# Performance work log

Measured on AMD Instinct MI355X. Metric: run time of the kernel, lower is better.

The kernel has to match this reference:

```python
import math
import jax, jax.numpy as jnp
import numpy as np

NUM_TIERS = 3
TIER_SIZE = 50
GT_FACTOR = 2.0
MAX_REL = 8  # upper bound on relevant (gt) docs per query; labels built to respect this
B, D = 4096, 1000


def diff_fn(x):
    # 'maxmargin': relu(1 - x)
    return jax.nn.relu(1.0 - x)


def get_tier_inds(num_negatives):
    # tier_distance is None -> auto-spread tier centers
    mids = math.ceil((num_negatives - 2 * TIER_SIZE) / (NUM_TIERS - 1))
    return [0] + [TIER_SIZE // 2 + i * mids for i in range(1, NUM_TIERS - 1)] + [num_negatives - TIER_SIZE]


def setup_inputs() -> dict:
    key = jax.random.key(0)
    k1, k2 = jax.random.split(key)
    scores = jax.random.normal(k1, (B, D), dtype=jnp.float32)
    # n_i relevant docs per query in [1, MAX_REL]; labels[i,:n_i] = positions, rest -1
    n = jax.random.randint(k2, (B,), 1, MAX_REL + 1)
    cols = jnp.arange(D)
    labels = jnp.where(cols[None, :] < n[:, None], cols[None, :], -1).astype(jnp.int32)
    return {"scores": scores, "labels": labels}


def reference(scores, labels):
    Bq, Dq = scores.shape
    start_inds = get_tier_inds(Dq)
    loss = jnp.zeros(Bq, dtype=jnp.float32)
    # tiered pairwise diffs: each tier vs everything below it
    for t in range(NUM_TIERS - 1):
        s1 = scores[:, start_inds[t]:start_inds[t] + TIER_SIZE]      # (B, tier_size)
        s2 = scores[:, start_inds[t + 1]:]                            # (B, rest)
        d = diff_fn(s1[:, :, None] - s2[:, None, :])                  # (B, tier_size, rest)
        loss = loss + jnp.sum(d, axis=(1, 2)) / (s1.shape[1] * s2.shape[1])
    # ground-truth component (gt_function='same'), vectorized with masks instead of per-row loop
    n = jnp.sum(labels > -1, axis=1)                                  # (B,) num relevant per query
    rel_mask = jnp.arange(MAX_REL)[None, :] < n[:, None]              # (B, MAX_REL): j < n_i
    neg_mask = jnp.arange(Dq)[None, :] >= n[:, None]                  # (B, D): k >= n_i
    d = diff_fn(scores[:, :MAX_REL, None] - scores[:, None, :])       # (B, MAX_REL, D)
    mask = rel_mask[:, :, None] & neg_mask[:, None, :]
    gt_loss = jnp.sum(jnp.where(mask, d, 0.0), axis=(1, 2)) / Dq      # (B,)
    loss = loss + GT_FACTOR * gt_loss
    return jnp.mean(loss)  # reduction='mean'
```

## Files before the change

kernel.cpp:

```cpp
#include <hip/hip_runtime.h>


#define BQ 4096
#define DQ 1000

__global__ __launch_bounds__(256) void mtl_row_kernel(const float* __restrict__ scores,
                                                      const int* __restrict__ labels,
                                                      float* __restrict__ row_loss) {
    const int row = blockIdx.x;
    __shared__ float s[DQ];
    __shared__ int n_sh;
    __shared__ float wsum[4];

    const float* sr = scores + (size_t)row * DQ;
    for (int j = threadIdx.x; j < DQ; j += 256) s[j] = sr[j];

    if (threadIdx.x == 0) {
        const int* lr = labels + (size_t)row * DQ;
        int n = 0;
        #pragma unroll
        for (int k = 0; k < 8; ++k) n += (lr[k] > -1) ? 1 : 0;
        n_sh = n;
    }
    __syncthreads();
    const int n = n_sh;

    float acc = 0.0f;
    for (int j = threadIdx.x; j < DQ; j += 256) {
        const float sj = s[j];
        if (j >= 475) {
            float t = 0.0f;
            #pragma unroll 10
            for (int i = 0; i < 50; ++i) t += fmaxf(1.0f - s[i] + sj, 0.0f);
            acc += t * (1.0f / 26250.0f);
        }
        if (j >= 950) {
            float t = 0.0f;
            #pragma unroll 10
            for (int i = 475; i < 525; ++i) t += fmaxf(1.0f - s[i] + sj, 0.0f);
            acc += t * (1.0f / 2500.0f);
        }
        if (j >= n) {
            float t = 0.0f;
            for (int k = 0; k < n; ++k) t += fmaxf(1.0f - s[k] + sj, 0.0f);
            acc += t * (2.0f / 1000.0f);
        }
    }

    #pragma unroll
    for (int off = 32; off > 0; off >>= 1) acc += __shfl_down(acc, off, 64);
    const int lane = threadIdx.x & 63;
    const int wid  = threadIdx.x >> 6;
    if (lane == 0) wsum[wid] = acc;
    __syncthreads();
    if (threadIdx.x == 0) row_loss[row] = wsum[0] + wsum[1] + wsum[2] + wsum[3];
}

__global__ __launch_bounds__(256) void mtl_reduce_kernel(const float* __restrict__ row_loss,
                                                         float* __restrict__ out) {
    __shared__ float wsum[4];
    float acc = 0.0f;
    for (int i = threadIdx.x; i < BQ; i += 256) acc += row_loss[i];
    #pragma unroll
    for (int off = 32; off > 0; off >>= 1) acc += __shfl_down(acc, off, 64);
    const int lane = threadIdx.x & 63;
    const int wid  = threadIdx.x >> 6;
    if (lane == 0) wsum[wid] = acc;
    __syncthreads();
    if (threadIdx.x == 0) out[0] = (wsum[0] + wsum[1] + wsum[2] + wsum[3]) * (1.0f / (float)BQ);
}

extern "C" void kernel_launch(void* const* d_in, const int* in_sizes, int n_in,
                              void* d_out, int out_size, void* d_ws, size_t ws_size,
                              hipStream_t stream) {
    const float* scores = (const float*)d_in[0];
    const int*   labels = (const int*)d_in[1];
    float* row_loss = (float*)d_ws;
    float* out = (float*)d_out;

    mtl_row_kernel<<<BQ, 256, 0, stream>>>(scores, labels, row_loss);
    mtl_reduce_kernel<<<1, 256, 0, stream>>>(row_loss, out);
}
```

Baseline: 92.33 us.

## Replace tier-0 pairwise hinge sum with sort, prefix sums and binary search

The 50 tier-0 scores are sorted with a rank-based sort in one wavefront and prefix-summed, so each of the 525 lower documents gets its hinge contribution from a binary search plus one prefix lookup instead of a 50-term loop. The remaining tier-1 and ground-truth work is redistributed across the other three wavefronts, and row loads use float4. This removes most of the O(50·525) arithmetic per row. In exchange it adds extra barriers, idle lanes during the sort, and a different float summation order.

```diff
diff --git a/kernel.cpp b/kernel.cpp
--- a/kernel.cpp
+++ b/kernel.cpp
@@ -1,4 +1,5 @@
 #include <hip/hip_runtime.h>
+#include <float.h>
 
 
 #define BQ 4096
@@ -7,15 +8,24 @@
 __global__ __launch_bounds__(256) void mtl_row_kernel(const float* __restrict__ scores,
                                                       const int* __restrict__ labels,
                                                       float* __restrict__ row_loss) {
-    const int row = blockIdx.x;
+    const int row  = blockIdx.x;
+    const int tid  = threadIdx.x;
+    const int lane = tid & 63;
+    const int wid  = tid >> 6;
+
     __shared__ float s[DQ];
-    __shared__ int n_sh;
+    __shared__ float sorted0[64];
+    __shared__ float pre0[65];
+    __shared__ int   n_sh;
     __shared__ float wsum[4];
 
     const float* sr = scores + (size_t)row * DQ;
-    for (int j = threadIdx.x; j < DQ; j += 256) s[j] = sr[j];
-
-    if (threadIdx.x == 0) {
+    if (tid < 250) {
+        float4 v = ((const float4*)sr)[tid];
+        s[tid * 4 + 0] = v.x; s[tid * 4 + 1] = v.y;
+        s[tid * 4 + 2] = v.z; s[tid * 4 + 3] = v.w;
+    }
+    if (tid == 0) {
         const int* lr = labels + (size_t)row * DQ;
         int n = 0;
         #pragma unroll
@@ -26,34 +36,69 @@
     const int n = n_sh;
 
     float acc = 0.0f;
-    for (int j = threadIdx.x; j < DQ; j += 256) {
-        const float sj = s[j];
-        if (j >= 475) {
-            float t = 0.0f;
-            #pragma unroll 10
-            for (int i = 0; i < 50; ++i) t += fmaxf(1.0f - s[i] + sj, 0.0f);
-            acc += t * (1.0f / 26250.0f);
+
+    if (wid == 0) {
+        if (lane >= 50) sorted0[lane] = FLT_MAX;
+        else {
+            float v = s[lane];
+            int rank = 0;
+            for (int k = 0; k < 50; ++k) {
+                float sk = s[k];
+                rank += (sk < v || (sk == v && k < lane)) ? 1 : 0;
+            }
+            sorted0[rank] = v;
         }
-        if (j >= 950) {
-            float t = 0.0f;
-            #pragma unroll 10
-            for (int i = 475; i < 525; ++i) t += fmaxf(1.0f - s[i] + sj, 0.0f);
-            acc += t * (1.0f / 2500.0f);
+    } else {
+        float sj = s[950 + (lane < 50 ? lane : 0)];
+        float t1 = 0.0f;
+        for (int i = wid - 1; i < 50; i += 3) {
+            float ri = s[475 + i];
+            t1 += fmaxf(1.0f - ri + sj, 0.0f);
         }
-        if (j >= n) {
-            float t = 0.0f;
-            for (int k = 0; k < n; ++k) t += fmaxf(1.0f - s[k] + sj, 0.0f);
-            acc += t * (2.0f / 1000.0f);
+        if (lane < 50) acc += t1 * (1.0f / 2500.0f);
+
+        float tgt = 0.0f;
+        for (int j = tid - 64; j < DQ; j += 192) {
+            if (j >= n) {
+                float x = 1.0f + s[j];
+                float t = 0.0f;
+                for (int k = 0; k < n; ++k)
+                    t += fmaxf(x - s[k], 0.0f);
+                tgt += t;
+            }
         }
+        acc += tgt * (2.0f / 1000.0f);
     }
+    __syncthreads();
+
+    if (wid == 0) {
+        float val = (lane < 50) ? sorted0[lane] : 0.0f;
+        #pragma unroll
+        for (int off = 1; off < 64; off <<= 1) {
+            float tmp = __shfl_up(val, off, 64);
+            if (lane >= off) val += tmp;
+        }
+        pre0[lane + 1] = val;
+        if (lane == 0) pre0[0] = 0.0f;
+    }
+    __syncthreads();
+
+    float t0 = 0.0f;
+    for (int j = 475 + tid; j < DQ; j += 256) {
+        float x = 1.0f + s[j];
+        int c = 0;
+        #pragma unroll
+        for (int st = 32; st >= 1; st >>= 1)
+            c += (sorted0[c + st - 1] < x) ? st : 0;
+        t0 += (float)c * x - pre0[c];
+    }
+    acc += t0 * (1.0f / 26250.0f);
 
     #pragma unroll
     for (int off = 32; off > 0; off >>= 1) acc += __shfl_down(acc, off, 64);
-    const int lane = threadIdx.x & 63;
-    const int wid  = threadIdx.x >> 6;
     if (lane == 0) wsum[wid] = acc;
     __syncthreads();
-    if (threadIdx.x == 0) row_loss[row] = wsum[0] + wsum[1] + wsum[2] + wsum[3];
+    if (tid == 0) row_loss[row] = wsum[0] + wsum[1] + wsum[2] + wsum[3];
 }
 
 __global__ __launch_bounds__(256) void mtl_reduce_kernel(const float* __restrict__ row_loss,
```

New measurement: 88.39 us. 4.3% less time.

## Replace tier pairwise loops with sorted prefix-sum relu sums, one wave per row

Applied to the files above, without the earlier changes.

Each wave now handles one row, holding the row in registers instead of shared memory. The two 50-element tier windows are sorted with a wave-level bitonic sort and prefix-summed. Each relu sum against a tier then becomes a binary search plus a count-times-value minus prefix lookup, replacing the 50-iteration inner loops. This removes most of the O(50·D) arithmetic and the block-level syncs, but adds shuffle-heavy sort, scan and search steps and hard-codes the tier boundaries into lane and register masks.

```diff
diff --git a/kernel.cpp b/kernel.cpp
--- a/kernel.cpp
+++ b/kernel.cpp
@@ -1,59 +1,107 @@
 #include <hip/hip_runtime.h>
+#include <float.h>
 
 
 #define BQ 4096
 #define DQ 1000
 
-__global__ __launch_bounds__(256) void mtl_row_kernel(const float* __restrict__ scores,
-                                                      const int* __restrict__ labels,
-                                                      float* __restrict__ row_loss) {
-    const int row = blockIdx.x;
-    __shared__ float s[DQ];
-    __shared__ int n_sh;
-    __shared__ float wsum[4];
+__device__ __forceinline__ float bitonic_sort64(float v, int lane) {
+    #pragma unroll
+    for (int size = 2; size <= 64; size <<= 1) {
+        #pragma unroll
+        for (int stride = size >> 1; stride > 0; stride >>= 1) {
+            float other = __shfl_xor(v, stride, 64);
+            bool keep_min = (((lane & stride) == 0) == ((lane & size) == 0));
+            v = keep_min ? fminf(v, other) : fmaxf(v, other);
+        }
+    }
+    return v;
+}
 
+__device__ __forceinline__ float excl_scan50(float sv, int lane) {
+    float x = (lane < 50) ? sv : 0.0f;
+    float inc = x;
+    #pragma unroll
+    for (int off = 1; off < 64; off <<= 1) {
+        float t = __shfl_up(inc, off, 64);
+        if (lane >= off) inc += t;
+    }
+    return inc - x;
+}
+
+__device__ __forceinline__ float sorted_relu_sum(float x, float sv, float pre) {
+    int c = 0;
+    #pragma unroll
+    for (int st = 32; st >= 1; st >>= 1) {
+        float scv = __shfl(sv, c + st - 1, 64);
+        c += (scv < x) ? st : 0;
+    }
+    float p = __shfl(pre, c, 64);
+    return (float)c * x - p;
+}
+
+__global__ __launch_bounds__(256) void mtl_rows(const float* __restrict__ scores,
+                                               const int* __restrict__ labels,
+                                               float* __restrict__ row_loss) {
+    const int tid  = threadIdx.x;
+    const int lane = tid & 63;
+    const int w    = tid >> 6;
+    const int row  = blockIdx.x * 4 + w;
     const float* sr = scores + (size_t)row * DQ;
-    for (int j = threadIdx.x; j < DQ; j += 256) s[j] = sr[j];
 
-    if (threadIdx.x == 0) {
-        const int* lr = labels + (size_t)row * DQ;
-        int n = 0;
+    float q[16];
+    #pragma unroll
+    for (int t = 0; t < 15; ++t) q[t] = sr[lane + 64 * t];
+    q[15] = (lane < 40) ? sr[960 + lane] : 0.0f;
+
+    int lv = -1;
+    if (lane < 8) lv = labels[(size_t)row * DQ + lane];
+    const int n = __popcll(__ballot(lv > -1));
+
+    float sv0  = bitonic_sort64((lane < 50) ? q[0] : FLT_MAX, lane);
+    float pre0 = excl_scan50(sv0, lane);
+
+    float r1 = FLT_MAX;
+    if (lane < 50) r1 = sr[475 + lane];
+    float sv1  = bitonic_sort64(r1, lane);
+    float pre1 = excl_scan50(sv1, lane);
+
+    float tgt[16];
+    #pragma unroll
+    for (int t = 0; t < 16; ++t) tgt[t] = 0.0f;
+    for (int k = 0; k < n; ++k) {
+        float gk = 1.0f - __shfl(q[0], k, 64);
         #pragma unroll
-        for (int k = 0; k < 8; ++k) n += (lr[k] > -1) ? 1 : 0;
-        n_sh = n;
+        for (int t = 0; t < 16; ++t) tgt[t] += fmaxf(q[t] + gk, 0.0f);
     }
-    __syncthreads();
-    const int n = n_sh;
+    float gts = (lane >= n) ? tgt[0] : 0.0f;
+    #pragma unroll
+    for (int t = 1; t < 15; ++t) gts += tgt[t];
+    gts += (lane < 40) ? tgt[15] : 0.0f;
+    float acc = gts * (2.0f / 1000.0f);
 
-    float acc = 0.0f;
-    for (int j = threadIdx.x; j < DQ; j += 256) {
-        const float sj = s[j];
-        if (j >= 475) {
-            float t = 0.0f;
-            #pragma unroll 10
-            for (int i = 0; i < 50; ++i) t += fmaxf(1.0f - s[i] + sj, 0.0f);
-            acc += t * (1.0f / 26250.0f);
-        }
-        if (j >= 950) {
-            float t = 0.0f;
-            #pragma unroll 10
-            for (int i = 475; i < 525; ++i) t += fmaxf(1.0f - s[i] + sj, 0.0f);
-            acc += t * (1.0f / 2500.0f);
-        }
-        if (j >= n) {
-            float t = 0.0f;
-            for (int k = 0; k < n; ++k) t += fmaxf(1.0f - s[k] + sj, 0.0f);
-            acc += t * (2.0f / 1000.0f);
-        }
+    float t0s = 0.0f;
+    #pragma unroll
+    for (int t = 7; t < 16; ++t) {
+        float x = 1.0f + q[t];
+        float val = sorted_relu_sum(x, sv0, pre0);
+        bool act = (t == 7) ? (lane >= 27)
+                 : (t == 15) ? (lane < 40)
+                 : true;
+        t0s += act ? val : 0.0f;
+    }
+    acc += t0s * (1.0f / 26250.0f);
+
+    {
+        float v14 = sorted_relu_sum(1.0f + q[14], sv1, pre1);
+        acc += (lane >= 54) ? v14 * (1.0f / 2500.0f) : 0.0f;
+        float v15 = sorted_relu_sum(1.0f + q[15], sv1, pre1);
+        acc += (lane < 40) ? v15 * (1.0f / 2500.0f) : 0.0f;
     }
 
     #pragma unroll
     for (int off = 32; off > 0; off >>= 1) acc += __shfl_down(acc, off, 64);
-    const int lane = threadIdx.x & 63;
-    const int wid  = threadIdx.x >> 6;
-    if (lane == 0) wsum[wid] = acc;
-    __syncthreads();
-    if (threadIdx.x == 0) row_loss[row] = wsum[0] + wsum[1] + wsum[2] + wsum[3];
+    if (lane == 0) row_loss[row] = acc;
 }
 
 __global__ __launch_bounds__(256) void mtl_reduce_kernel(const float* __restrict__ row_loss,
@@ -78,6 +126,6 @@
     float* row_loss = (float*)d_ws;
     float* out = (float*)d_out;
 
-    mtl_row_kernel<<<BQ, 256, 0, stream>>>(scores, labels, row_loss);
+    mtl_rows<<<BQ / 4, 256, 0, stream>>>(scores, labels, row_loss);
     mtl_reduce_kernel<<<1, 256, 0, stream>>>(row_loss, out);
 }
```

New measurement: 83.58 us. 1.1x faster.
